# Kernel optimization log

Measured on AMD Instinct MI355X. Metric: run time of the kernel, lower is better.

Reference implementation:

```python
import jax, jax.numpy as jnp
import numpy as np

H = 1024
B, S = 8, 2048
EPS = 1e-5


def _layernorm(x, w, b):
    m = jnp.mean(x, axis=-1, keepdims=True)
    v = jnp.mean((x - m) ** 2, axis=-1, keepdims=True)
    return (x - m) * jax.lax.rsqrt(v + EPS) * w + b


def setup_inputs() -> dict:
    key = jax.random.key(0)
    ks = jax.random.split(key, 10)
    x = jax.random.normal(ks[0], (B, S, H), dtype=jnp.float32)
    # LayerNorm params (torch default init: weight=1, bias=0)
    qn_w = jnp.ones((H,), jnp.float32)
    qn_b = jnp.zeros((H,), jnp.float32)
    kvn_w = jnp.ones((H,), jnp.float32)
    kvn_b = jnp.zeros((H,), jnp.float32)
    # q_prime/k_prime/v_prime ~ U(-0.5, 0.5)
    q_prime = jax.random.uniform(ks[1], (1, H), jnp.float32) - 0.5
    k_prime = jax.random.uniform(ks[2], (1, H), jnp.float32) - 0.5
    v_prime = jax.random.uniform(ks[3], (1, H), jnp.float32) - 0.5
    # Linear params, torch-style fan_in init
    lim = 1.0 / np.sqrt(H)
    qW = jax.random.uniform(ks[4], (H, H), jnp.float32, -lim, lim)
    qb = jax.random.uniform(ks[5], (H,), jnp.float32, -lim, lim)
    v1W = jax.random.uniform(ks[6], (H, H), jnp.float32, -lim, lim)
    v1b = jax.random.uniform(ks[7], (H,), jnp.float32, -lim, lim)
    v2W = jax.random.uniform(ks[8], (H, H), jnp.float32, -lim, lim)
    v2b = jax.random.uniform(ks[9], (H,), jnp.float32, -lim, lim)
    return {"x": x, "qn_w": qn_w, "qn_b": qn_b, "kvn_w": kvn_w, "kvn_b": kvn_b,
            "q_prime": q_prime, "k_prime": k_prime, "v_prime": v_prime,
            "qW": qW, "qb": qb, "v1W": v1W, "v1b": v1b, "v2W": v2W, "v2b": v2b}


def reference(x, qn_w, qn_b, kvn_w, kvn_b, q_prime, k_prime, v_prime,
              qW, qb, v1W, v1b, v2W, v2b):
    divisor = jnp.sqrt(jnp.float32(x.shape[-1]))
    xqn = _layernorm(x, qn_w, qn_b)            # [B,S,H]
    xkvn = _layernorm(x, kvn_w, kvn_b)         # [B,S,H]
    kr = xkvn * jax.nn.sigmoid(k_prime)        # [B,S,H]
    qr = (xqn @ qW.T + qb) * jax.nn.sigmoid(q_prime)  # [B,S,H]
    vp = jax.nn.sigmoid(v_prime)               # [1,H]
    gate = jax.nn.sigmoid(vp @ v1W.T + v1b) * jnp.tanh(vp @ v2W.T + v2b)  # [1,H]
    vr = xkvn * gate                           # [B,S,H]
    scores = jnp.einsum('bsh,bth->bst', qr, kr) / divisor  # [B,S,S]
    b, s, t = scores.shape
    # global softmax over flattened seq x seq matrix
    attn = jax.nn.softmax(scores.reshape(b, s * t), axis=-1).reshape(b, s, t)
    attended = jnp.einsum('bst,bth->bsh', attn, vr)
    return attended + xqn
```

## Files before the change

### kernel.cpp

```cpp
#include <hip/hip_runtime.h>
#include <stdint.h>


#define DEVI __device__ __forceinline__

typedef __bf16 bf16x8 __attribute__((ext_vector_type(8)));
typedef float  f32x4  __attribute__((ext_vector_type(4)));

typedef __attribute__((address_space(3))) uint32_t lds_u32_t;
typedef __attribute__((address_space(1))) uint32_t glb_u32_t;

DEVI uint16_t f2bf(float f) {
  union { float f; uint32_t u; } v; v.f = f;
  uint32_t r = (v.u + 0x7fffu + ((v.u >> 16) & 1u)) >> 16;
  return (uint16_t)r;
}
DEVI float bf2f(uint16_t b) {
  union { uint32_t u; float f; } v; v.u = ((uint32_t)b) << 16;
  return v.f;
}
DEVI float sigm(float x) { return 1.0f / (1.0f + __expf(-x)); }

DEVI void gl_lds16(const void* g, const void* lds_base) {
  __builtin_amdgcn_global_load_lds((glb_u32_t*)(uintptr_t)g,
                                   (lds_u32_t*)(uint32_t)(uintptr_t)lds_base,
                                   16, 0, 0);
}


#define SLOT (256 * 32)

DEVI void stage_half(const uint16_t* __restrict__ src, size_t ld, int kbase,
                     uint16_t* slot, int tid) {
#pragma unroll
  for (int q = 0; q < 2; q++) {
    const int idx = q * 512 + tid;
    const int r = idx >> 2;
    const int cl = (((idx & 3) ^ ((r >> 1) & 3)) * 8);
    gl_lds16(src + (size_t)r * ld + (kbase + cl),
             slot + (size_t)(q * 512 + (tid & ~63)) * 8);
  }
}

DEVI void gemm256(const uint16_t* __restrict__ A, size_t lda,
                  const uint16_t* __restrict__ B, size_t ldb,
                  int K, uint16_t* sA, uint16_t* sB, f32x4 (&acc)[8][4])
{
  const int tid = threadIdx.x, lane = tid & 63, w = tid >> 6;
  const int wr = (w >> 2) * 128, wc = (w & 3) * 64;
  const int m16 = lane & 15, quad = lane >> 4;
  const int NT = K >> 6, NH = K >> 5;

  stage_half(B, ldb, 0, sB, tid);
  stage_half(A, lda, 0, sA, tid);
  stage_half(B, ldb, 32, sB + SLOT, tid);
  stage_half(A, lda, 32, sA + SLOT, tid);
  stage_half(B, ldb, 64, sB + 2 * SLOT, tid);
  stage_half(A, lda, 64, sA + 2 * SLOT, tid);
  asm volatile("s_waitcnt vmcnt(4)" ::: "memory");
  __builtin_amdgcn_s_barrier();

  const int sw = (quad ^ ((m16 >> 1) & 3)) * 8;

  for (int t = 0; t < NT; t++) {
#pragma unroll
    for (int ks = 0; ks < 2; ks++) {
      const uint16_t* a_s = sA + ((2 * t + ks) & 3) * SLOT;
      const uint16_t* b_s = sB + ((2 * t + ks) & 3) * SLOT;
      const int h = 2 * t + 3 + ks;

      bf16x8 bv[4], af[4];
#pragma unroll
      for (int i = 0; i < 4; i++)
        bv[i] = *(const bf16x8*)(b_s + (wc + i * 16 + m16) * 32 + sw);
#pragma unroll
      for (int i = 0; i < 4; i++)
        af[i] = *(const bf16x8*)(a_s + (wr + i * 16 + m16) * 32 + sw);
      if (h < NH) stage_half(B, ldb, h * 32, sB + (h & 3) * SLOT, tid);
      __builtin_amdgcn_s_barrier();
      __builtin_amdgcn_s_setprio(1);
#pragma unroll
      for (int mi = 0; mi < 4; mi++)
#pragma unroll
        for (int ni = 0; ni < 4; ni++)
          acc[mi][ni] = __builtin_amdgcn_mfma_f32_16x16x32_bf16(
              af[mi], bv[ni], acc[mi][ni], 0, 0, 0);
      __builtin_amdgcn_s_setprio(0);

      bf16x8 af2[4];
#pragma unroll
      for (int i = 0; i < 4; i++)
        af2[i] = *(const bf16x8*)(a_s + (wr + 64 + i * 16 + m16) * 32 + sw);
      if (h < NH) stage_half(A, lda, h * 32, sA + (h & 3) * SLOT, tid);
      if (ks == 1) {
        if (t < NT - 2) asm volatile("s_waitcnt vmcnt(4)" ::: "memory");
        else            asm volatile("s_waitcnt vmcnt(0)" ::: "memory");
      }
      __builtin_amdgcn_s_barrier();
      __builtin_amdgcn_s_setprio(1);
#pragma unroll
      for (int mi = 0; mi < 4; mi++)
#pragma unroll
        for (int ni = 0; ni < 4; ni++)
          acc[4 + mi][ni] = __builtin_amdgcn_mfma_f32_16x16x32_bf16(
              af2[mi], bv[ni], acc[4 + mi][ni], 0, 0, 0);
      __builtin_amdgcn_s_setprio(0);
    }
  }
}

__global__ void gate_kernel(const float* __restrict__ v_prime,
                            const float* __restrict__ v1W, const float* __restrict__ v1b,
                            const float* __restrict__ v2W, const float* __restrict__ v2b,
                            const float* __restrict__ k_prime,
                            float* __restrict__ gate2)
{
  const int tid = threadIdx.x, lane = tid & 63, w = tid >> 6;
  const int j = blockIdx.x * 4 + w;
  float d1 = 0.f, d2 = 0.f;
  for (int it = 0; it < 16; it++) {
    int i = it * 64 + lane;
    float vp = sigm(v_prime[i]);
    d1 += vp * v1W[(size_t)j * 1024 + i];
    d2 += vp * v2W[(size_t)j * 1024 + i];
  }
  for (int off = 32; off; off >>= 1) { d1 += __shfl_xor(d1, off); d2 += __shfl_xor(d2, off); }
  if (lane == 0)
    gate2[j] = sigm(d1 + v1b[j]) * tanhf(d2 + v2b[j]) / sigm(k_prime[j]);
}

__global__ void cvt_kernel(const float* __restrict__ src, uint16_t* __restrict__ dst)
{
  size_t i = ((size_t)blockIdx.x * 256 + threadIdx.x) * 4;
  float4 v = *(const float4*)(src + i);
  *(ushort4*)(dst + i) = make_ushort4(f2bf(v.x), f2bf(v.y), f2bf(v.z), f2bf(v.w));
}

__global__ __launch_bounds__(256) void ln_kernel(
    const float* __restrict__ x,
    const float* __restrict__ qn_w, const float* __restrict__ qn_b,
    const float* __restrict__ kvn_w, const float* __restrict__ kvn_b,
    const float* __restrict__ k_prime,
    uint16_t* __restrict__ xqn_bf, uint16_t* __restrict__ kr,
    float* __restrict__ krowsq)
{
  const int lane = threadIdx.x & 63, w = threadIdx.x >> 6;
  const int row = blockIdx.x * 4 + w;
  const float4* xr = (const float4*)(x + (size_t)row * 1024);
  float4 v[4];
  float s = 0.f, sq = 0.f;
#pragma unroll
  for (int i = 0; i < 4; i++) {
    v[i] = xr[i * 64 + lane];
    s  += v[i].x + v[i].y + v[i].z + v[i].w;
    sq += v[i].x * v[i].x + v[i].y * v[i].y + v[i].z * v[i].z + v[i].w * v[i].w;
  }
  for (int off = 32; off; off >>= 1) { s += __shfl_xor(s, off); sq += __shfl_xor(sq, off); }
  const float mean = s * (1.f / 1024.f);
  const float rstd = rsqrtf(sq * (1.f / 1024.f) - mean * mean + 1e-5f);

  float ksq = 0.f;
  const size_t o4 = (size_t)row * 256;
#pragma unroll
  for (int i = 0; i < 4; i++) {
    const int idx = i * 64 + lane;
    float4 qw = ((const float4*)qn_w)[idx],  qb4 = ((const float4*)qn_b)[idx];
    float4 kw = ((const float4*)kvn_w)[idx], kb4 = ((const float4*)kvn_b)[idx];
    float4 kp = ((const float4*)k_prime)[idx];
    float xn0 = (v[i].x - mean) * rstd, xn1 = (v[i].y - mean) * rstd;
    float xn2 = (v[i].z - mean) * rstd, xn3 = (v[i].w - mean) * rstd;
    float xq0 = xn0 * qw.x + qb4.x, xq1 = xn1 * qw.y + qb4.y;
    float xq2 = xn2 * qw.z + qb4.z, xq3 = xn3 * qw.w + qb4.w;
    float xk0 = xn0 * kw.x + kb4.x, xk1 = xn1 * kw.y + kb4.y;
    float xk2 = xn2 * kw.z + kb4.z, xk3 = xn3 * kw.w + kb4.w;
    float k0 = xk0 * sigm(kp.x), k1 = xk1 * sigm(kp.y);
    float k2 = xk2 * sigm(kp.z), k3 = xk3 * sigm(kp.w);
    ksq += k0 * k0 + k1 * k1 + k2 * k2 + k3 * k3;
    ((ushort4*)xqn_bf)[o4 + idx] = make_ushort4(f2bf(xq0), f2bf(xq1), f2bf(xq2), f2bf(xq3));
    ((ushort4*)kr)[o4 + idx] = make_ushort4(f2bf(k0), f2bf(k1), f2bf(k2), f2bf(k3));
  }
  for (int off = 32; off; off >>= 1) ksq += __shfl_xor(ksq, off);
  if (lane == 0) krowsq[row] = ksq;
}

__global__ __launch_bounds__(512, 2) void qr_gemm_kernel(
    const uint16_t* __restrict__ xqn_bf, const uint16_t* __restrict__ qWbf,
    const float* __restrict__ qb, const float* __restrict__ q_prime,
    uint16_t* __restrict__ qr, float* __restrict__ qnormsq)
{
  __shared__ uint16_t sA[4 * SLOT], sB[4 * SLOT];
  const int lid = blockIdx.x;
  const int c = lid >> 6, r = lid & 63;
  f32x4 acc[8][4];
#pragma unroll
  for (int i = 0; i < 8; i++)
#pragma unroll
    for (int j = 0; j < 4; j++) acc[i][j] = (f32x4)0.0f;

  gemm256(xqn_bf + (size_t)r * 256 * 1024, 1024,
          qWbf + (size_t)c * 256 * 1024, 1024, 1024, sA, sB, acc);

  const int tid = threadIdx.x, lane = tid & 63, w = tid >> 6;
  const int m16 = lane & 15, quad = lane >> 4;
  const int rbase = r * 256 + (w >> 2) * 128, cbase = c * 256 + (w & 3) * 64;
#pragma unroll
  for (int ai = 0; ai < 8; ai++) {
    const int gr0 = rbase + (ai >> 2) * 64 + (ai & 3) * 16 + quad * 4;
    float rsq[4] = {0.f, 0.f, 0.f, 0.f};
#pragma unroll
    for (int ni = 0; ni < 4; ni++) {
      const int gc = cbase + ni * 16 + m16;
      const float scale = sigm(q_prime[gc]);
      const float bias = qb[gc];
#pragma unroll
      for (int rr = 0; rr < 4; rr++) {
        float val = (acc[ai][ni][rr] + bias) * scale;
        qr[(size_t)(gr0 + rr) * 1024 + gc] = f2bf(val);
        rsq[rr] += val * val;
      }
    }
#pragma unroll
    for (int rr = 0; rr < 4; rr++) {
      float tq = rsq[rr];
      tq += __shfl_xor(tq, 1); tq += __shfl_xor(tq, 2);
      tq += __shfl_xor(tq, 4); tq += __shfl_xor(tq, 8);
      if (m16 == 0) atomicAdd(&qnormsq[gr0 + rr], tq);
    }
  }
}

__global__ void bound_kernel(const float* __restrict__ qnormsq,
                             const float* __restrict__ krowsq, float* __restrict__ MZ)
{
  const int b = blockIdx.x, tid = threadIdx.x, lane = tid & 63, w = tid >> 6;
  float mq = 0.f, mk = 0.f;
  for (int i = tid; i < 2048; i += 256) {
    mq = fmaxf(mq, qnormsq[b * 2048 + i]);
    mk = fmaxf(mk, krowsq[b * 2048 + i]);
  }
  for (int off = 32; off; off >>= 1) {
    mq = fmaxf(mq, __shfl_xor(mq, off));
    mk = fmaxf(mk, __shfl_xor(mk, off));
  }
  __shared__ float rm[4], rk[4];
  if (lane == 0) { rm[w] = mq; rk[w] = mk; }
  __syncthreads();
  if (tid == 0) {
    float qmax = fmaxf(fmaxf(rm[0], rm[1]), fmaxf(rm[2], rm[3]));
    float kmax = fmaxf(fmaxf(rk[0], rk[1]), fmaxf(rk[2], rk[3]));
    MZ[b] = sqrtf(qmax * kmax) * 0.03125f;
  }
}

__global__ void transpose_kernel(const uint16_t* __restrict__ kr,
                                 const float* __restrict__ gate2,
                                 uint16_t* __restrict__ vrt)
{
  __shared__ uint16_t t[64 * 72];
  const int b = blockIdx.z;
  const int t0 = blockIdx.x * 64, h0 = blockIdx.y * 64;
  const uint16_t* src = kr + (size_t)b * 2048 * 1024;
#pragma unroll
  for (int p = 0; p < 2; p++) {
    int flat = p * 256 + threadIdx.x;
    int r = flat >> 3, c = (flat & 7) * 8;
    *(uint4*)(&t[r * 72 + c]) = *(const uint4*)(src + (size_t)(t0 + r) * 1024 + h0 + c);
  }
  __syncthreads();
  uint16_t* dst = vrt + (size_t)b * 1024 * 2048;
#pragma unroll
  for (int p = 0; p < 2; p++) {
    int flat = p * 256 + threadIdx.x;
    int oh = flat >> 3, oc = (flat & 7) * 8;
    const float g = gate2[h0 + oh];
    union { uint16_t e[8]; uint4 v; } u;
#pragma unroll
    for (int j = 0; j < 8; j++) u.e[j] = f2bf(bf2f(t[(oc + j) * 72 + oh]) * g);
    *(uint4*)(dst + (size_t)(h0 + oh) * 2048 + t0 + oc) = u.v;
  }
}

__global__ __launch_bounds__(512, 2) void scores_kernel(
    const uint16_t* __restrict__ qr, const uint16_t* __restrict__ kr,
    const float* __restrict__ MZ,
    uint16_t* __restrict__ scores, float* __restrict__ blockZ)
{
  __shared__ uint16_t sA[4 * SLOT], sB[4 * SLOT];
  __shared__ float redz[8];
  const int lid = blockIdx.x;
  const int b = lid >> 6, c = (lid >> 3) & 7, r = lid & 7;
  f32x4 acc[8][4];
#pragma unroll
  for (int i = 0; i < 8; i++)
#pragma unroll
    for (int j = 0; j < 4; j++) acc[i][j] = (f32x4)0.0f;

  gemm256(qr + (size_t)b * 2048 * 1024 + (size_t)r * 256 * 1024, 1024,
          kr + (size_t)b * 2048 * 1024 + (size_t)c * 256 * 1024, 1024,
          1024, sA, sB, acc);

  const float Mhat = MZ[b];
  const int tid = threadIdx.x, lane = tid & 63, w = tid >> 6;
  const int m16 = lane & 15, quad = lane >> 4;
  const int rbase = r * 256 + (w >> 2) * 128, cbase = c * 256 + (w & 3) * 64;
  uint16_t* S = scores + ((size_t)b << 22);
  float zt = 0.f;
#pragma unroll
  for (int ai = 0; ai < 8; ai++) {
    const int gr0 = rbase + (ai >> 2) * 64 + (ai & 3) * 16 + quad * 4;
#pragma unroll
    for (int ni = 0; ni < 4; ni++) {
      const int gc = cbase + ni * 16 + m16;
#pragma unroll
      for (int rr = 0; rr < 4; rr++) {
        float pe = __expf(acc[ai][ni][rr] * 0.03125f - Mhat);
        zt += pe;
        S[(size_t)(gr0 + rr) * 2048 + gc] = f2bf(pe);
      }
    }
  }
  for (int off = 32; off; off >>= 1) zt += __shfl_xor(zt, off);
  if (lane == 0) redz[w] = zt;
  __syncthreads();
  if (tid == 0) {
    float sz = 0.f;
#pragma unroll
    for (int i = 0; i < 8; i++) sz += redz[i];
    blockZ[lid] = sz;
  }
}

__global__ void zreduce_kernel(const float* __restrict__ blockZ, float* __restrict__ MZ)
{
  const int b = blockIdx.x, lane = threadIdx.x;
  float z = blockZ[b * 64 + lane];
  for (int off = 32; off; off >>= 1) z += __shfl_xor(z, off);
  if (lane == 0) MZ[8 + b] = z;
}

__global__ __launch_bounds__(512, 2) void pv_gemm_kernel(
    const uint16_t* __restrict__ P, const uint16_t* __restrict__ vrt,
    const float* __restrict__ MZ, const uint16_t* __restrict__ xqn_bf,
    float* __restrict__ out)
{
  __shared__ uint16_t sA[4 * SLOT], sB[4 * SLOT];
  const int lid = blockIdx.x;
  const int b = lid >> 5, c = (lid >> 3) & 3, r = lid & 7;
  f32x4 acc[8][4];
#pragma unroll
  for (int i = 0; i < 8; i++)
#pragma unroll
    for (int j = 0; j < 4; j++) acc[i][j] = (f32x4)0.0f;

  gemm256(P + ((size_t)b << 22) + (size_t)r * 256 * 2048, 2048,
          vrt + (size_t)b * 1024 * 2048 + (size_t)c * 256 * 2048, 2048,
          2048, sA, sB, acc);

  const float invZ = 1.0f / MZ[8 + b];
  const int tid = threadIdx.x, lane = tid & 63, w = tid >> 6;
  const int m16 = lane & 15, quad = lane >> 4;
  const int rbase = r * 256 + (w >> 2) * 128, cbase = c * 256 + (w & 3) * 64;
#pragma unroll
  for (int ai = 0; ai < 8; ai++) {
    const int gr0 = rbase + (ai >> 2) * 64 + (ai & 3) * 16 + quad * 4;
#pragma unroll
    for (int ni = 0; ni < 4; ni++) {
      const int gc = cbase + ni * 16 + m16;
#pragma unroll
      for (int rr = 0; rr < 4; rr++) {
        size_t o = ((size_t)b * 2048 + gr0 + rr) * 1024 + gc;
        out[o] = acc[ai][ni][rr] * invZ + bf2f(xqn_bf[o]);
      }
    }
  }
}

extern "C" void kernel_launch(void* const* d_in, const int* in_sizes, int n_in,
                              void* d_out, int out_size, void* d_ws, size_t ws_size,
                              hipStream_t stream) {
  const float* x       = (const float*)d_in[0];
  const float* qn_w    = (const float*)d_in[1];
  const float* qn_b    = (const float*)d_in[2];
  const float* kvn_w   = (const float*)d_in[3];
  const float* kvn_b   = (const float*)d_in[4];
  const float* q_prime = (const float*)d_in[5];
  const float* k_prime = (const float*)d_in[6];
  const float* v_prime = (const float*)d_in[7];
  const float* qW      = (const float*)d_in[8];
  const float* qb      = (const float*)d_in[9];
  const float* v1W     = (const float*)d_in[10];
  const float* v1b     = (const float*)d_in[11];
  const float* v2W     = (const float*)d_in[12];
  const float* v2b     = (const float*)d_in[13];
  float* out = (float*)d_out;

  const size_t BS = 16384, H = 1024;
  char* ws = (char*)d_ws;
  size_t off = 0;
  auto alloc = [&](size_t bytes) -> char* {
    char* p = ws + off;
    off = (off + bytes + 255) & ~(size_t)255;
    return p;
  };
  float*    gate2   = (float*)alloc(H * 4);
  float*    MZ      = (float*)alloc(16 * 4);
  float*    blockZ  = (float*)alloc(2048 * 4);
  float*    qnormsq = (float*)alloc(16384 * 4);
  float*    krowsq  = (float*)alloc(16384 * 4);
  uint16_t* qWbf    = (uint16_t*)alloc(H * H * 2);
  uint16_t* xqn_bf  = (uint16_t*)alloc(BS * H * 2);
  uint16_t* kr      = (uint16_t*)alloc(BS * H * 2);
  uint16_t* scores  = (uint16_t*)alloc(BS * H * 2 * 2);
  uint16_t* vrt     = (uint16_t*)alloc(BS * H * 2);
  uint16_t* qr      = (uint16_t*)alloc(BS * H * 2);

  hipMemsetAsync(qnormsq, 0, 16384 * 4, stream);
  gate_kernel<<<256, 256, 0, stream>>>(v_prime, v1W, v1b, v2W, v2b, k_prime, gate2);
  cvt_kernel<<<1024, 256, 0, stream>>>(qW, qWbf);
  ln_kernel<<<4096, 256, 0, stream>>>(x, qn_w, qn_b, kvn_w, kvn_b, k_prime,
                                      xqn_bf, kr, krowsq);
  qr_gemm_kernel<<<256, 512, 0, stream>>>(xqn_bf, qWbf, qb, q_prime, qr, qnormsq);
  transpose_kernel<<<dim3(32, 16, 8), 256, 0, stream>>>(kr, gate2, vrt);
  bound_kernel<<<8, 256, 0, stream>>>(qnormsq, krowsq, MZ);
  scores_kernel<<<512, 512, 0, stream>>>(qr, kr, MZ, scores, blockZ);
  zreduce_kernel<<<8, 64, 0, stream>>>(blockZ, MZ);
  pv_gemm_kernel<<<256, 512, 0, stream>>>(scores, vrt, MZ, xqn_bf, out);
}
```

Baseline: 367.5 us.

## Restructure GEMM main loop into four MFMA quadrants with interleaved loads

Restructures the 256x256 bf16 GEMM inner loop. Each 64-wide K tile is now handled as four MFMA quadrants (A-top/A-bottom by B-left/B-right), and each quadrant covers both 32-wide K halves. LDS fragment reads and global-to-LDS staging are interleaved between quadrants, with barriers, lgkmcnt waits and sched_barriers placed around each MFMA burst. The aim is to cut register pressure from fragment loads and overlap LDS reads with MFMA work. In exchange there are more barriers per iteration, and the prefetch ordering changes, which must still respect the 4-slot ring.

After: 370.2 us. Within noise of the previous version (+0.7%).

```diff
diff --git a/kernel.cpp b/kernel.cpp
--- a/kernel.cpp
+++ b/kernel.cpp
@@ -42,6 +42,24 @@
   }
 }
 
+#define MFMA_QUAD(AARR, BARR, GOFF, NOFF)                                   \
+  __builtin_amdgcn_s_barrier();                                             \
+  asm volatile("s_waitcnt lgkmcnt(0)" ::: "memory");                        \
+  __builtin_amdgcn_sched_barrier(0);                                        \
+  __builtin_amdgcn_s_setprio(1);                                            \
+  _Pragma("unroll")                                                         \
+  for (int ks = 0; ks < 2; ks++)                                            \
+    _Pragma("unroll")                                                       \
+    for (int mi = 0; mi < 4; mi++)                                          \
+      _Pragma("unroll")                                                     \
+      for (int nj = 0; nj < 2; nj++)                                        \
+        acc[(GOFF) + mi][(NOFF) + nj] =                                     \
+            __builtin_amdgcn_mfma_f32_16x16x32_bf16(                        \
+                AARR[ks * 4 + mi], BARR[ks * 2 + nj],                       \
+                acc[(GOFF) + mi][(NOFF) + nj], 0, 0, 0);                    \
+  __builtin_amdgcn_s_setprio(0);                                            \
+  __builtin_amdgcn_s_barrier();
+
 DEVI void gemm256(const uint16_t* __restrict__ A, size_t lda,
                   const uint16_t* __restrict__ B, size_t ldb,
                   int K, uint16_t* sA, uint16_t* sB, f32x4 (&acc)[8][4])
@@ -50,6 +68,7 @@
   const int wr = (w >> 2) * 128, wc = (w & 3) * 64;
   const int m16 = lane & 15, quad = lane >> 4;
   const int NT = K >> 6, NH = K >> 5;
+  const int sw = (quad ^ ((m16 >> 1) & 3)) * 8;
 
   stage_half(B, ldb, 0, sB, tid);
   stage_half(A, lda, 0, sA, tid);
@@ -60,52 +79,47 @@
   asm volatile("s_waitcnt vmcnt(4)" ::: "memory");
   __builtin_amdgcn_s_barrier();
 
-  const int sw = (quad ^ ((m16 >> 1) & 3)) * 8;
-
   for (int t = 0; t < NT; t++) {
+    const uint16_t* aks[2] = { sA + ((2 * t) & 3) * SLOT, sA + ((2 * t + 1) & 3) * SLOT };
+    const uint16_t* bks[2] = { sB + ((2 * t) & 3) * SLOT, sB + ((2 * t + 1) & 3) * SLOT };
+    bf16x8 a0[8], a1[8], b0[4], b1[4];
+
 #pragma unroll
     for (int ks = 0; ks < 2; ks++) {
-      const uint16_t* a_s = sA + ((2 * t + ks) & 3) * SLOT;
-      const uint16_t* b_s = sB + ((2 * t + ks) & 3) * SLOT;
-      const int h = 2 * t + 3 + ks;
-
-      bf16x8 bv[4], af[4];
 #pragma unroll
       for (int i = 0; i < 4; i++)
-        bv[i] = *(const bf16x8*)(b_s + (wc + i * 16 + m16) * 32 + sw);
+        a0[ks * 4 + i] = *(const bf16x8*)(aks[ks] + (wr + i * 16 + m16) * 32 + sw);
+#pragma unroll
+      for (int j = 0; j < 2; j++)
+        b0[ks * 2 + j] = *(const bf16x8*)(bks[ks] + (wc + j * 16 + m16) * 32 + sw);
+    }
+    if (2 * t + 3 < NH)
+      stage_half(B, ldb, (2 * t + 3) * 32, sB + ((2 * t + 3) & 3) * SLOT, tid);
+    MFMA_QUAD(a0, b0, 0, 0)
+
+#pragma unroll
+    for (int ks = 0; ks < 2; ks++)
+#pragma unroll
+      for (int j = 0; j < 2; j++)
+        b1[ks * 2 + j] = *(const bf16x8*)(bks[ks] + (wc + 32 + j * 16 + m16) * 32 + sw);
+    if (2 * t + 3 < NH)
+      stage_half(A, lda, (2 * t + 3) * 32, sA + ((2 * t + 3) & 3) * SLOT, tid);
+    MFMA_QUAD(a0, b1, 0, 2)
+
+#pragma unroll
+    for (int ks = 0; ks < 2; ks++)
 #pragma unroll
       for (int i = 0; i < 4; i++)
-        af[i] = *(const bf16x8*)(a_s + (wr + i * 16 + m16) * 32 + sw);
-      if (h < NH) stage_half(B, ldb, h * 32, sB + (h & 3) * SLOT, tid);
-      __builtin_amdgcn_s_barrier();
-      __builtin_amdgcn_s_setprio(1);
-#pragma unroll
-      for (int mi = 0; mi < 4; mi++)
-#pragma unroll
-        for (int ni = 0; ni < 4; ni++)
-          acc[mi][ni] = __builtin_amdgcn_mfma_f32_16x16x32_bf16(
-              af[mi], bv[ni], acc[mi][ni], 0, 0, 0);
-      __builtin_amdgcn_s_setprio(0);
-
-      bf16x8 af2[4];
-#pragma unroll
-      for (int i = 0; i < 4; i++)
-        af2[i] = *(const bf16x8*)(a_s + (wr + 64 + i * 16 + m16) * 32 + sw);
-      if (h < NH) stage_half(A, lda, h * 32, sA + (h & 3) * SLOT, tid);
-      if (ks == 1) {
-        if (t < NT - 2) asm volatile("s_waitcnt vmcnt(4)" ::: "memory");
-        else            asm volatile("s_waitcnt vmcnt(0)" ::: "memory");
-      }
-      __builtin_amdgcn_s_barrier();
-      __builtin_amdgcn_s_setprio(1);
-#pragma unroll
-      for (int mi = 0; mi < 4; mi++)
-#pragma unroll
-        for (int ni = 0; ni < 4; ni++)
-          acc[4 + mi][ni] = __builtin_amdgcn_mfma_f32_16x16x32_bf16(
-              af2[mi], bv[ni], acc[4 + mi][ni], 0, 0, 0);
-      __builtin_amdgcn_s_setprio(0);
-    }
+        a1[ks * 4 + i] = *(const bf16x8*)(aks[ks] + (wr + 64 + i * 16 + m16) * 32 + sw);
+    if (2 * t + 4 < NH)
+      stage_half(B, ldb, (2 * t + 4) * 32, sB + ((2 * t + 4) & 3) * SLOT, tid);
+    MFMA_QUAD(a1, b1, 4, 2)
+
+    if (2 * t + 4 < NH)
+      stage_half(A, lda, (2 * t + 4) * 32, sA + ((2 * t + 4) & 3) * SLOT, tid);
+    if (t < NT - 2) asm volatile("s_waitcnt vmcnt(4)" ::: "memory");
+    else            asm volatile("s_waitcnt vmcnt(0)" ::: "memory");
+    MFMA_QUAD(a1, b0, 4, 0)
   }
 }
 
```
